# Performance work log

Measured on AMD Instinct MI355X. Metric: run time of the kernel, lower is better.

## Reference

```python
import jax, jax.numpy as jnp
import numpy as np
import itertools

NODE_DIM = 30
NUM_FEAT = 64
EDGE_DIM = NODE_DIM * NODE_DIM  # 900
D_IN, HID, LAT = 1024, 2048, 256
OUT_DIM = EDGE_DIM + NODE_DIM * NUM_FEAT  # 2820

_opt_nodes = [20, 21, 22, 23, 24, 25, 26, 27, 28, 29]
_opt_edges = [(i, j) for i, j in itertools.product(_opt_nodes, _opt_nodes) if i <= j]  # 55
_log_nodes = [20, 21, 22, 23, 24, 25, 26, 27, 28, 29, 14, 15]
_log_edges = [(i, j) for i, j in itertools.product(_log_nodes, _log_nodes) if i <= j]  # 78
N_OPT_NODES = len(_opt_nodes)          # 10
N_OPT_EDGES = len(_opt_edges)          # 55
N_LOG_NODES = len(_log_nodes)          # 12 (softmax width; only first 10 applied)
N_LOG_EDGES = len(_log_edges)          # 78 (softmax width; only first 55 applied)
OPT_NODES = jnp.array(_opt_nodes)
E0 = jnp.array([e[0] for e in _opt_edges])
E1 = jnp.array([e[1] for e in _opt_edges])


def _bn(x, g, b, m, v):
    # eval-mode BatchNorm1d, eps=1e-5
    return (x - m) * jax.lax.rsqrt(v + 1e-5) * g + b


def _attn_mlp(x, W1, b1, W2, b2):
    return jnp.tanh(x @ W1 + b1) @ W2 + b2


def _apply_attention(node_repr, edge_repr, node_w, edge_w):
    # softmax over full weight width, but indices always come from the optical lists
    nw = jax.nn.softmax(node_w, axis=1)[:, :N_OPT_NODES]   # [B,10]
    ew = jax.nn.softmax(edge_w, axis=1)[:, :N_OPT_EDGES]   # [B,55]
    node_repr = node_repr.at[:, OPT_NODES, :].set(node_repr[:, OPT_NODES, :] * nw[:, :, None])
    edge_repr = edge_repr.at[:, E0, E1].set(edge_repr[:, E0, E1] * ew)
    return node_repr, edge_repr


def setup_inputs() -> dict:
    key = jax.random.key(0)
    ks = iter(jax.random.split(key, 64))
    B = 8192
    s = 0.02
    def W(shape):
        return jax.random.normal(next(ks), shape, dtype=jnp.float32) * s
    inp = {
        "x": jax.random.normal(next(ks), (B, D_IN), dtype=jnp.float32),
        "optical": jax.random.normal(next(ks), (B, D_IN), dtype=jnp.float32),
        "log": jax.random.normal(next(ks), (B, D_IN), dtype=jnp.float32),
        "enc_W": W((D_IN, HID)), "enc_b": W((HID,)),
        "bn1_g": jnp.ones((HID,)), "bn1_b": jnp.zeros((HID,)),
        "bn1_m": W((HID,)), "bn1_v": jax.random.uniform(next(ks), (HID,)) + 0.5,
        "mu_W": W((HID, LAT)), "mu_b": W((LAT,)),
        "lv_W": W((HID, LAT)), "lv_b": W((LAT,)),
        "dec_W1": W((LAT, HID)), "dec_b1": W((HID,)),
        "bn2_g": jnp.ones((HID,)), "bn2_b": jnp.zeros((HID,)),
        "bn2_m": W((HID,)), "bn2_v": jax.random.uniform(next(ks), (HID,)) + 0.5,
        "dec_W2": W((HID, OUT_DIM)), "dec_b2": W((OUT_DIM,)),
        "on_W1": W((D_IN, D_IN // 2)), "on_b1": W((D_IN // 2,)),
        "on_W2": W((D_IN // 2, N_OPT_NODES)), "on_b2": W((N_OPT_NODES,)),
        "oe_W1": W((D_IN, D_IN // 2)), "oe_b1": W((D_IN // 2,)),
        "oe_W2": W((D_IN // 2, N_OPT_EDGES)), "oe_b2": W((N_OPT_EDGES,)),
        "ln_W1": W((D_IN, D_IN // 2)), "ln_b1": W((D_IN // 2,)),
        "ln_W2": W((D_IN // 2, N_LOG_NODES)), "ln_b2": W((N_LOG_NODES,)),
        "le_W1": W((D_IN, D_IN // 2)), "le_b1": W((D_IN // 2,)),
        "le_W2": W((D_IN // 2, N_LOG_EDGES)), "le_b2": W((N_LOG_EDGES,)),
    }
    return inp


def reference(x, optical, log, enc_W, enc_b, bn1_g, bn1_b, bn1_m, bn1_v,
              mu_W, mu_b, lv_W, lv_b, dec_W1, dec_b1, bn2_g, bn2_b, bn2_m, bn2_v,
              dec_W2, dec_b2, on_W1, on_b1, on_W2, on_b2, oe_W1, oe_b1, oe_W2, oe_b2,
              ln_W1, ln_b1, ln_W2, ln_b2, le_W1, le_b1, le_W2, le_b2):
    # encode (Linear -> ReLU -> BatchNorm(eval) -> Dropout(identity))
    h1 = _bn(jax.nn.relu(x @ enc_W + enc_b), bn1_g, bn1_b, bn1_m, bn1_v)
    mu = h1 @ mu_W + mu_b
    logvar = h1 @ lv_W + lv_b
    z = mu  # eval-mode reparameterize
    # decode
    h2 = _bn(jax.nn.relu(z @ dec_W1 + dec_b1), bn2_g, bn2_b, bn2_m, bn2_v)
    out = h2 @ dec_W2 + dec_b2
    edge_repr = out[:, :EDGE_DIM].reshape(-1, NODE_DIM, NODE_DIM)
    node_repr = out[:, EDGE_DIM:].reshape(-1, NODE_DIM, NUM_FEAT)
    # optical attention
    onw = _attn_mlp(optical, on_W1, on_b1, on_W2, on_b2)
    oew = _attn_mlp(optical, oe_W1, oe_b1, oe_W2, oe_b2)
    node_repr, edge_repr = _apply_attention(node_repr, edge_repr, onw, oew)
    # log attention (wider softmax, same indices — faithful to original code)
    lnw = _attn_mlp(log, ln_W1, ln_b1, ln_W2, ln_b2)
    lew = _attn_mlp(log, le_W1, le_b1, le_W2, le_b2)
    node_repr, edge_repr = _apply_attention(node_repr, edge_repr, lnw, lew)
    return edge_repr, node_repr, mu, logvar
```

## Files before the change

kernel.cpp:

```cpp
#include <hip/hip_runtime.h>

using u16 = unsigned short;
using u32 = unsigned int;

typedef __attribute__((ext_vector_type(8))) short bf16x8;
typedef __attribute__((ext_vector_type(4))) float f32x4;

#define MFMA16 __builtin_amdgcn_mfma_f32_16x16x32_bf16

__device__ __forceinline__ u16 f2bf(float f) {
  u32 u = __float_as_uint(f);
  u += 0x7fffu + ((u >> 16) & 1u);
  return (u16)(u >> 16);
}
__device__ __forceinline__ float bf2f(u16 h) { return __uint_as_float(((u32)h) << 16); }

__device__ __forceinline__ void gld16(const u16* g, u16* s) {
  __builtin_amdgcn_global_load_lds((const __attribute__((address_space(1))) u32*)g,
                                   (__attribute__((address_space(3))) u32*)s, 16, 0, 0);
}

struct EpParams {
  const float* bias;
  const float* bias2;
  const u16* b2;
  const float* bnsc;
  const float* bnsh;
  u16* dhi; u16* dlo; int dstride;
  float* f32a; float* f32b; int f32stride;
  const float* nscale; const float* escale;
};

template<int EP, int NM, bool SLO>
__global__ __launch_bounds__(256, (NM == 1) ? 3 : 2) void gemm_k(
    const u16* __restrict__ Ah, const u16* __restrict__ Al, int lda,
    const u16* __restrict__ Bh, const u16* __restrict__ Bl,
    int K, int N, EpParams p)
{
  __shared__ __align__(16) u16 sAh[4096], sBh[4096];
  __shared__ __align__(16) u16 sAl[(NM >= 2) ? 4096 : 16];
  __shared__ __align__(16) u16 sBl[(NM == 3) ? 4096 : 16];
  const int t = threadIdx.x;
  const int lane = t & 63, wid = t >> 6;
  const int tm = blockIdx.x, tn = blockIdx.y;

  const u16* BhS = Bh;
  const float* bias = p.bias;
  if constexpr (EP == 2 || EP == 5) {
    if (tm >= 64) { BhS = p.b2; bias = p.bias2; }
  }

  const int rp = t >> 2, sp = t & 3;
  const int rl = (rp & ~1) | ((rp & 1) ^ ((rp >> 2) & 1));
  const int sl = sp ^ (rl & 3);
  const u16* pAh = Ah + (size_t)(tm * 128 + rl) * (size_t)lda + sl * 8;
  const u16* pBh = BhS + (size_t)(tn * 128 + rl) * (size_t)K + sl * 8;
  const u16* pAl = (NM >= 2) ? Al + (size_t)(tm * 128 + rl) * (size_t)lda + sl * 8 : pAh;
  const u16* pBl = (NM == 3) ? Bl + (size_t)(tn * 128 + rl) * (size_t)K + sl * 8 : pBh;
  const size_t aStep = (size_t)64 * (size_t)lda;
  const size_t bStep = (size_t)64 * (size_t)K;

  f32x4 acc[4][4];
#pragma unroll
  for (int m = 0; m < 4; m++)
#pragma unroll
    for (int n = 0; n < 4; n++) acc[m][n] = f32x4{0.f, 0.f, 0.f, 0.f};

  const int fr = lane & 15, fg = lane >> 4;
  const int wm = wid >> 1, wn = wid & 1;

  for (int kk = 0; kk < K; kk += 32) {
    gld16(pAh + kk,          sAh + wid * 512);
    gld16(pAh + aStep + kk,  sAh + 2048 + wid * 512);
    gld16(pBh + kk,          sBh + wid * 512);
    gld16(pBh + bStep + kk,  sBh + 2048 + wid * 512);
    if constexpr (NM >= 2) {
      gld16(pAl + kk,         sAl + wid * 512);
      gld16(pAl + aStep + kk, sAl + 2048 + wid * 512);
    }
    if constexpr (NM == 3) {
      gld16(pBl + kk,         sBl + wid * 512);
      gld16(pBl + bStep + kk, sBl + 2048 + wid * 512);
    }
    __syncthreads();

    bf16x8 a_h[4], b_h[4], a_l[4], b_l[4];
#pragma unroll
    for (int f = 0; f < 4; f++) {
      const int ar = wm * 64 + f * 16 + fr;
      const int br = wn * 64 + f * 16 + fr;
      a_h[f] = *(const bf16x8*)&sAh[(ar * 32 + fg * 8) ^ ((ar & 7) << 3)];
      b_h[f] = *(const bf16x8*)&sBh[(br * 32 + fg * 8) ^ ((br & 7) << 3)];
      if constexpr (NM >= 2) a_l[f] = *(const bf16x8*)&sAl[(ar * 32 + fg * 8) ^ ((ar & 7) << 3)];
      if constexpr (NM == 3) b_l[f] = *(const bf16x8*)&sBl[(br * 32 + fg * 8) ^ ((br & 7) << 3)];
    }
#pragma unroll
    for (int m = 0; m < 4; m++)
#pragma unroll
      for (int n = 0; n < 4; n++) {
        if constexpr (NM == 3)
          acc[m][n] = MFMA16(a_h[m], b_l[n], acc[m][n], 0, 0, 0);
        if constexpr (NM >= 2)
          acc[m][n] = MFMA16(a_l[m], b_h[n], acc[m][n], 0, 0, 0);
        acc[m][n] = MFMA16(a_h[m], b_h[n], acc[m][n], 0, 0, 0);
      }
    __syncthreads();
  }

  const int rowb = tm * 128 + wm * 64;
  const int colb = tn * 128 + wn * 64;
#pragma unroll
  for (int n = 0; n < 4; n++) {
    const int col = colb + n * 16 + fr;
#pragma unroll
    for (int m = 0; m < 4; m++) {
#pragma unroll
      for (int r = 0; r < 4; r++) {
        const int row = rowb + m * 16 + fg * 4 + r;
        float val = acc[m][n][r];
        if constexpr (EP == 0) {
          val += bias[col];
          val = fmaxf(val, 0.f);
          val = val * p.bnsc[col] + p.bnsh[col];
          u16 h = f2bf(val);
          p.dhi[(size_t)row * p.dstride + col] = h;
          if constexpr (SLO)
            p.dlo[(size_t)row * p.dstride + col] = f2bf(val - bf2f(h));
        } else if constexpr (EP == 1) {
          val += bias[col];
          if (col < 256) {
            p.f32a[(size_t)row * 256 + col] = val;
            u16 h = f2bf(val);
            p.dhi[(size_t)row * 256 + col] = h;
            p.dlo[(size_t)row * 256 + col] = f2bf(val - bf2f(h));
          } else {
            p.f32b[(size_t)row * 256 + (col - 256)] = val;
          }
        } else if constexpr (EP == 2) {
          val = tanhf(val + bias[col]);
          p.dhi[(size_t)row * p.dstride + col] = f2bf(val);
        } else if constexpr (EP == 5) {
          if (tm < 64) {
            if (col < 65) p.f32a[(size_t)row * 65 + col] = val + bias[col];
          } else {
            if (col < 90) p.f32b[(size_t)(row - 8192) * 90 + col] = val + bias[col];
          }
        } else {
          if (col < N) {
            val += bias[col];
            if (col < 900) {
              int rr = col / 30, cc = col - rr * 30;
              float s = 1.f;
              if (rr >= 20 && cc >= 20 && rr <= cc) {
                int i0 = rr - 20, j0 = cc - 20;
                int k = i0 * 10 - ((i0 * (i0 - 1)) >> 1) + (j0 - i0);
                s = p.escale[(size_t)row * 55 + k];
              }
              p.f32a[(size_t)row * 900 + col] = val * s;
            } else {
              int tc = col - 900, rr = tc >> 6;
              float s = (rr >= 20) ? p.nscale[(size_t)row * 10 + (rr - 20)] : 1.f;
              p.f32b[(size_t)row * 1920 + tc] = val * s;
            }
          }
        }
      }
    }
  }
}

__global__ void conv3(const float* __restrict__ x, const float* __restrict__ opt,
                      const float* __restrict__ lg, u16* __restrict__ xh,
                      u16* __restrict__ xl, u16* __restrict__ oh, u16* __restrict__ lh) {
  const int SEG = 8192 * 1024 / 4;
  int i = blockIdx.x * blockDim.x + threadIdx.x;
  if (i < SEG) {
    float4 v = ((const float4*)x)[i];
    ushort4 hh, ll;
    hh.x = f2bf(v.x); ll.x = f2bf(v.x - bf2f(hh.x));
    hh.y = f2bf(v.y); ll.y = f2bf(v.y - bf2f(hh.y));
    hh.z = f2bf(v.z); ll.z = f2bf(v.z - bf2f(hh.z));
    hh.w = f2bf(v.w); ll.w = f2bf(v.w - bf2f(hh.w));
    ((ushort4*)xh)[i] = hh;
    ((ushort4*)xl)[i] = ll;
  } else if (i < 2 * SEG) {
    int j = i - SEG;
    float4 v = ((const float4*)opt)[j];
    ushort4 hh;
    hh.x = f2bf(v.x); hh.y = f2bf(v.y); hh.z = f2bf(v.z); hh.w = f2bf(v.w);
    ((ushort4*)oh)[j] = hh;
  } else if (i < 3 * SEG) {
    int j = i - 2 * SEG;
    float4 v = ((const float4*)lg)[j];
    ushort4 hh;
    hh.x = f2bf(v.x); hh.y = f2bf(v.y); hh.z = f2bf(v.z); hh.w = f2bf(v.w);
    ((ushort4*)lh)[j] = hh;
  }
}

struct WTJob { const float* src; u16* dh; int K, N, nbx, blk0; };
struct WTJobs { WTJob j[9]; };
__global__ void conv_wT_all(WTJobs J) {
  __shared__ float tile[32][33];
  const int b = blockIdx.x;
  int ji = 0;
#pragma unroll
  for (int q = 1; q < 9; q++) if (b >= J.j[q].blk0) ji = q;
  const WTJob jb = J.j[ji];
  const int bl = b - jb.blk0;
  const int kb = bl % jb.nbx, nb = bl / jb.nbx;
  const int k0 = kb * 32, n0 = nb * 32;
  const int tx = threadIdx.x, ty = threadIdx.y;
#pragma unroll
  for (int i = ty; i < 32; i += 8) {
    int n = n0 + tx;
    tile[i][tx] = (n < jb.N) ? jb.src[(size_t)(k0 + i) * jb.N + n] : 0.f;
  }
  __syncthreads();
#pragma unroll
  for (int i = ty; i < 32; i += 8) {
    int n = n0 + i, k = k0 + tx;
    jb.dh[(size_t)n * jb.K + k] = f2bf(tile[tx][i]);
  }
}

__global__ void conv_w2bd(const float* __restrict__ Wa, int Na,
                          const float* __restrict__ Wb, int Nb,
                          u16* __restrict__ Th) {
  int idx = blockIdx.x * blockDim.x + threadIdx.x;
  if (idx >= 128 * 1024) return;
  int n = idx >> 10, k = idx & 1023;
  float v = 0.f;
  if (n < Na) { if (k < 512) v = Wa[(size_t)k * Na + n]; }
  else if (n < Na + Nb) { if (k >= 512) v = Wb[(size_t)(k - 512) * Nb + (n - Na)]; }
  Th[idx] = f2bf(v);
}

struct PrepArgs {
  const float *bn1_g, *bn1_b, *bn1_m, *bn1_v, *bn2_g, *bn2_b, *bn2_m, *bn2_v;
  const float *mu_b, *lv_b, *on_b1, *oe_b1, *ln_b1, *le_b1, *on_b2, *oe_b2, *ln_b2, *le_b2;
  float *bn1sc, *bn1sh, *bn2sc, *bn2sh, *bias_mulv, *bias_o1, *bias_l1, *bias_o2, *bias_l2;
};
__global__ void prep_k(PrepArgs a) {
  int i = blockIdx.x * blockDim.x + threadIdx.x;
  if (i < 2048) {
    float s = a.bn1_g[i] * rsqrtf(a.bn1_v[i] + 1e-5f);
    a.bn1sc[i] = s; a.bn1sh[i] = a.bn1_b[i] - a.bn1_m[i] * s;
  } else if (i < 4096) {
    int j = i - 2048;
    float s = a.bn2_g[j] * rsqrtf(a.bn2_v[j] + 1e-5f);
    a.bn2sc[j] = s; a.bn2sh[j] = a.bn2_b[j] - a.bn2_m[j] * s;
  } else if (i < 4608) {
    int j = i - 4096; a.bias_mulv[j] = (j < 256) ? a.mu_b[j] : a.lv_b[j - 256];
  } else if (i < 5632) {
    int j = i - 4608; a.bias_o1[j] = (j < 512) ? a.on_b1[j] : a.oe_b1[j - 512];
  } else if (i < 6656) {
    int j = i - 5632; a.bias_l1[j] = (j < 512) ? a.ln_b1[j] : a.le_b1[j - 512];
  } else if (i < 6721) {
    int j = i - 6656; a.bias_o2[j] = (j < 10) ? a.on_b2[j] : a.oe_b2[j - 10];
  } else if (i < 6811) {
    int j = i - 6721; a.bias_l2[j] = (j < 12) ? a.ln_b2[j] : a.le_b2[j - 12];
  }
}

__global__ void softmax_combine(const float* __restrict__ lo, const float* __restrict__ ll,
                                float* __restrict__ nsc, float* __restrict__ esc) {
  int b = blockIdx.x * blockDim.x + threadIdx.x;
  if (b >= 8192) return;
  const float* po = lo + (size_t)b * 65;
  const float* pl = ll + (size_t)b * 90;
  float mo = po[0];
  for (int i = 1; i < 10; i++) mo = fmaxf(mo, po[i]);
  float so = 0.f;
  for (int i = 0; i < 10; i++) so += expf(po[i] - mo);
  float ml = pl[0];
  for (int i = 1; i < 12; i++) ml = fmaxf(ml, pl[i]);
  float sl = 0.f;
  for (int i = 0; i < 12; i++) sl += expf(pl[i] - ml);
  float invn = 1.f / (so * sl);
  for (int i = 0; i < 10; i++)
    nsc[(size_t)b * 10 + i] = expf(po[i] - mo) * expf(pl[i] - ml) * invn;
  const float* qo = po + 10;
  const float* ql = pl + 12;
  float meo = qo[0];
  for (int i = 1; i < 55; i++) meo = fmaxf(meo, qo[i]);
  float seo = 0.f;
  for (int i = 0; i < 55; i++) seo += expf(qo[i] - meo);
  float mel = ql[0];
  for (int i = 1; i < 78; i++) mel = fmaxf(mel, ql[i]);
  float sel = 0.f;
  for (int i = 0; i < 78; i++) sel += expf(ql[i] - mel);
  float inve = 1.f / (seo * sel);
  for (int k = 0; k < 55; k++)
    esc[(size_t)b * 55 + k] = expf(qo[k] - meo) * expf(ql[k] - mel) * inve;
}

extern "C" void kernel_launch(void* const* d_in, const int* in_sizes, int n_in,
                              void* d_out, int out_size, void* d_ws, size_t ws_size,
                              hipStream_t stream) {
  const float* x       = (const float*)d_in[0];
  const float* optical = (const float*)d_in[1];
  const float* logx    = (const float*)d_in[2];
  const float* enc_W   = (const float*)d_in[3];
  const float* enc_b   = (const float*)d_in[4];
  const float* bn1_g   = (const float*)d_in[5];
  const float* bn1_b   = (const float*)d_in[6];
  const float* bn1_m   = (const float*)d_in[7];
  const float* bn1_v   = (const float*)d_in[8];
  const float* mu_W    = (const float*)d_in[9];
  const float* mu_b    = (const float*)d_in[10];
  const float* lv_W    = (const float*)d_in[11];
  const float* lv_b    = (const float*)d_in[12];
  const float* dec_W1  = (const float*)d_in[13];
  const float* dec_b1  = (const float*)d_in[14];
  const float* bn2_g   = (const float*)d_in[15];
  const float* bn2_b   = (const float*)d_in[16];
  const float* bn2_m   = (const float*)d_in[17];
  const float* bn2_v   = (const float*)d_in[18];
  const float* dec_W2  = (const float*)d_in[19];
  const float* dec_b2  = (const float*)d_in[20];
  const float* on_W1   = (const float*)d_in[21];
  const float* on_b1   = (const float*)d_in[22];
  const float* on_W2   = (const float*)d_in[23];
  const float* on_b2   = (const float*)d_in[24];
  const float* oe_W1   = (const float*)d_in[25];
  const float* oe_b1   = (const float*)d_in[26];
  const float* oe_W2   = (const float*)d_in[27];
  const float* oe_b2   = (const float*)d_in[28];
  const float* ln_W1   = (const float*)d_in[29];
  const float* ln_b1   = (const float*)d_in[30];
  const float* ln_W2   = (const float*)d_in[31];
  const float* ln_b2   = (const float*)d_in[32];
  const float* le_W1   = (const float*)d_in[33];
  const float* le_b1   = (const float*)d_in[34];
  const float* le_W2   = (const float*)d_in[35];
  const float* le_b2   = (const float*)d_in[36];

  const int B = 8192;
  float* out_edge = (float*)d_out;
  float* out_node = out_edge + (size_t)B * 900;
  float* out_mu   = out_node + (size_t)B * 1920;
  float* out_lv   = out_mu + (size_t)B * 256;

  char* base = (char*)d_ws;
  size_t off = 0;
  auto takeB = [&](size_t elems) -> u16* {
    u16* p = (u16*)(base + off);
    off = (off + elems * 2 + 255) & ~(size_t)255;
    return p;
  };
  auto takeF = [&](size_t elems) -> float* {
    float* p = (float*)(base + off);
    off = (off + elems * 4 + 255) & ~(size_t)255;
    return p;
  };
  u16* wEncH  = takeB(2048 * 1024);
  u16* wMulvH = takeB(512 * 2048);
  u16* wDec1H = takeB(2048 * 256);
  u16* wDec2H = takeB(2944 * 2048);
  u16* wO1H   = takeB(1024 * 1024);
  u16* wL1H   = takeB(1024 * 1024);
  u16* wO2H   = takeB(128 * 1024);
  u16* wL2H   = takeB(128 * 1024);
  u16* aXh = takeB((size_t)B * 1024); u16* aXl = takeB((size_t)B * 1024);
  u16* aOLh = takeB((size_t)2 * B * 1024);
  u16* aOh = aOLh;
  u16* aLh = aOLh + (size_t)B * 1024;
  u16* aHh = takeB((size_t)B * 2048); u16* aHl = takeB((size_t)B * 2048);
  u16* aZh = takeB((size_t)B * 256);  u16* aZl = takeB((size_t)B * 256);
  u16* aTh = takeB((size_t)2 * B * 1024);
  float* logitsO = takeF((size_t)B * 65);
  float* logitsL = takeF((size_t)B * 90);
  float* nsc = takeF((size_t)B * 10);
  float* esc = takeF((size_t)B * 55);
  float* bn1sc = takeF(2048); float* bn1sh = takeF(2048);
  float* bn2sc = takeF(2048); float* bn2sh = takeF(2048);
  float* bias_mulv = takeF(512);
  float* bias_o1 = takeF(1024);
  float* bias_l1 = takeF(1024);
  float* bias_o2 = takeF(65);
  float* bias_l2 = takeF(90);

  PrepArgs pa;
  pa.bn1_g = bn1_g; pa.bn1_b = bn1_b; pa.bn1_m = bn1_m; pa.bn1_v = bn1_v;
  pa.bn2_g = bn2_g; pa.bn2_b = bn2_b; pa.bn2_m = bn2_m; pa.bn2_v = bn2_v;
  pa.mu_b = mu_b; pa.lv_b = lv_b;
  pa.on_b1 = on_b1; pa.oe_b1 = oe_b1; pa.ln_b1 = ln_b1; pa.le_b1 = le_b1;
  pa.on_b2 = on_b2; pa.oe_b2 = oe_b2; pa.ln_b2 = ln_b2; pa.le_b2 = le_b2;
  pa.bn1sc = bn1sc; pa.bn1sh = bn1sh; pa.bn2sc = bn2sc; pa.bn2sh = bn2sh;
  pa.bias_mulv = bias_mulv; pa.bias_o1 = bias_o1; pa.bias_l1 = bias_l1;
  pa.bias_o2 = bias_o2; pa.bias_l2 = bias_l2;
  prep_k<<<27, 256, 0, stream>>>(pa);

  conv3<<<24576, 256, 0, stream>>>(x, optical, logx, aXh, aXl, aOh, aLh);

  WTJobs wj;
  int blk = 0;
  auto addjob = [&](int idx, const float* src, u16* dh, int K, int N, int Npad) {
    wj.j[idx] = WTJob{src, dh, K, N, K / 32, blk};
    blk += (K / 32) * (Npad / 32);
  };
  addjob(0, enc_W,  wEncH,  1024, 2048, 2048);
  addjob(1, mu_W,   wMulvH, 2048, 256, 256);
  addjob(2, lv_W,   wMulvH + (size_t)256 * 2048, 2048, 256, 256);
  addjob(3, dec_W1, wDec1H, 256, 2048, 2048);
  addjob(4, dec_W2, wDec2H, 2048, 2820, 2944);
  addjob(5, on_W1,  wO1H,                        1024, 512, 512);
  addjob(6, oe_W1,  wO1H + (size_t)512 * 1024,   1024, 512, 512);
  addjob(7, ln_W1,  wL1H,                        1024, 512, 512);
  addjob(8, le_W1,  wL1H + (size_t)512 * 1024,   1024, 512, 512);
  conv_wT_all<<<blk, dim3(32, 8), 0, stream>>>(wj);
  conv_w2bd<<<512, 256, 0, stream>>>(on_W2, 10, oe_W2, 55, wO2H);
  conv_w2bd<<<512, 256, 0, stream>>>(ln_W2, 12, le_W2, 78, wL2H);

  EpParams p;

  p = EpParams{};
  p.bias = enc_b; p.bnsc = bn1sc; p.bnsh = bn1sh;
  p.dhi = aHh; p.dlo = aHl; p.dstride = 2048;
  gemm_k<0, 2, true><<<dim3(64, 16), 256, 0, stream>>>(
      aXh, aXl, 1024, wEncH, nullptr, 1024, 2048, p);

  p = EpParams{};
  p.bias = bias_mulv; p.f32a = out_mu; p.f32b = out_lv;
  p.dhi = aZh; p.dlo = aZl; p.dstride = 256;
  gemm_k<1, 2, false><<<dim3(64, 4), 256, 0, stream>>>(
      aHh, aHl, 2048, wMulvH, nullptr, 2048, 512, p);

  p = EpParams{};
  p.bias = dec_b1; p.bnsc = bn2sc; p.bnsh = bn2sh;
  p.dhi = aHh; p.dlo = nullptr; p.dstride = 2048;
  gemm_k<0, 2, false><<<dim3(64, 16), 256, 0, stream>>>(
      aZh, aZl, 256, wDec1H, nullptr, 256, 2048, p);

  p = EpParams{};
  p.bias = bias_o1; p.bias2 = bias_l1; p.b2 = wL1H;
  p.dhi = aTh; p.dstride = 1024;
  gemm_k<2, 1, false><<<dim3(128, 8), 256, 0, stream>>>(
      aOLh, nullptr, 1024, wO1H, nullptr, 1024, 1024, p);

  p = EpParams{};
  p.bias = bias_o2; p.bias2 = bias_l2; p.b2 = wL2H;
  p.f32a = logitsO; p.f32b = logitsL;
  gemm_k<5, 1, false><<<dim3(128, 1), 256, 0, stream>>>(
      aTh, nullptr, 1024, wO2H, nullptr, 1024, 128, p);

  softmax_combine<<<32, 256, 0, stream>>>(logitsO, logitsL, nsc, esc);

  p = EpParams{};
  p.bias = dec_b2; p.nscale = nsc; p.escale = esc;
  p.f32a = out_edge; p.f32b = out_node;
  gemm_k<4, 1, false><<<dim3(64, 23), 256, 0, stream>>>(
      aHh, nullptr, 2048, wDec2H, nullptr, 2048, 2820, p);
}
```

Before: 786.0 us.

## Merge prep kernels and co-schedule independent GEMMs in combined launches

Folds the input conversion, weight transposes, block-diagonal weight packing and bias/BN prep into a single launch. It also runs independent GEMMs inside one grid: the encoder with the first attention MLP layer, mu/logvar with the second attention layer, and decoder layer 1 with the softmax. The goal is to cut launch overhead and fill the GPU with work from independent stages at the same time. The cost is that the combined kernels always allocate three LDS buffers and use a shared launch-bounds setting, which may reduce occupancy for the single-matrix GEMM paths.

```diff
diff --git a/kernel.cpp b/kernel.cpp
--- a/kernel.cpp
+++ b/kernel.cpp
@@ -31,32 +31,34 @@
   const float* nscale; const float* escale;
 };
 
+struct GemmJob {
+  const u16* Ah; const u16* Al; int lda;
+  const u16* Bh;
+  int K, N, ntm;
+  EpParams p;
+};
+
 template<int EP, int NM, bool SLO>
-__global__ __launch_bounds__(256, (NM == 1) ? 3 : 2) void gemm_k(
-    const u16* __restrict__ Ah, const u16* __restrict__ Al, int lda,
-    const u16* __restrict__ Bh, const u16* __restrict__ Bl,
-    int K, int N, EpParams p)
-{
-  __shared__ __align__(16) u16 sAh[4096], sBh[4096];
-  __shared__ __align__(16) u16 sAl[(NM >= 2) ? 4096 : 16];
-  __shared__ __align__(16) u16 sBl[(NM == 3) ? 4096 : 16];
+__device__ __forceinline__ void gemm_body(const GemmJob& J, int lbid,
+                                          u16* sAh, u16* sBh, u16* sAl) {
+  const EpParams& p = J.p;
   const int t = threadIdx.x;
   const int lane = t & 63, wid = t >> 6;
-  const int tm = blockIdx.x, tn = blockIdx.y;
-
-  const u16* BhS = Bh;
+  const int tm = lbid % J.ntm, tn = lbid / J.ntm;
+  const int K = J.K, lda = J.lda;
+
+  const u16* BhS = J.Bh;
   const float* bias = p.bias;
   if constexpr (EP == 2 || EP == 5) {
-    if (tm >= 64) { BhS = p.b2; bias = p.bias2; }
+    if (tm >= (J.ntm >> 1)) { BhS = p.b2; bias = p.bias2; }
   }
 
   const int rp = t >> 2, sp = t & 3;
   const int rl = (rp & ~1) | ((rp & 1) ^ ((rp >> 2) & 1));
   const int sl = sp ^ (rl & 3);
-  const u16* pAh = Ah + (size_t)(tm * 128 + rl) * (size_t)lda + sl * 8;
+  const u16* pAh = J.Ah + (size_t)(tm * 128 + rl) * (size_t)lda + sl * 8;
   const u16* pBh = BhS + (size_t)(tn * 128 + rl) * (size_t)K + sl * 8;
-  const u16* pAl = (NM >= 2) ? Al + (size_t)(tm * 128 + rl) * (size_t)lda + sl * 8 : pAh;
-  const u16* pBl = (NM == 3) ? Bl + (size_t)(tn * 128 + rl) * (size_t)K + sl * 8 : pBh;
+  const u16* pAl = (NM >= 2) ? J.Al + (size_t)(tm * 128 + rl) * (size_t)lda + sl * 8 : pAh;
   const size_t aStep = (size_t)64 * (size_t)lda;
   const size_t bStep = (size_t)64 * (size_t)K;
 
@@ -78,13 +80,9 @@
       gld16(pAl + kk,         sAl + wid * 512);
       gld16(pAl + aStep + kk, sAl + 2048 + wid * 512);
     }
-    if constexpr (NM == 3) {
-      gld16(pBl + kk,         sBl + wid * 512);
-      gld16(pBl + bStep + kk, sBl + 2048 + wid * 512);
-    }
     __syncthreads();
 
-    bf16x8 a_h[4], b_h[4], a_l[4], b_l[4];
+    bf16x8 a_h[4], b_h[4], a_l[4];
 #pragma unroll
     for (int f = 0; f < 4; f++) {
       const int ar = wm * 64 + f * 16 + fr;
@@ -92,14 +90,11 @@
       a_h[f] = *(const bf16x8*)&sAh[(ar * 32 + fg * 8) ^ ((ar & 7) << 3)];
       b_h[f] = *(const bf16x8*)&sBh[(br * 32 + fg * 8) ^ ((br & 7) << 3)];
       if constexpr (NM >= 2) a_l[f] = *(const bf16x8*)&sAl[(ar * 32 + fg * 8) ^ ((ar & 7) << 3)];
-      if constexpr (NM == 3) b_l[f] = *(const bf16x8*)&sBl[(br * 32 + fg * 8) ^ ((br & 7) << 3)];
     }
 #pragma unroll
     for (int m = 0; m < 4; m++)
 #pragma unroll
       for (int n = 0; n < 4; n++) {
-        if constexpr (NM == 3)
-          acc[m][n] = MFMA16(a_h[m], b_l[n], acc[m][n], 0, 0, 0);
         if constexpr (NM >= 2)
           acc[m][n] = MFMA16(a_l[m], b_h[n], acc[m][n], 0, 0, 0);
         acc[m][n] = MFMA16(a_h[m], b_h[n], acc[m][n], 0, 0, 0);
@@ -146,7 +141,7 @@
             if (col < 90) p.f32b[(size_t)(row - 8192) * 90 + col] = val + bias[col];
           }
         } else {
-          if (col < N) {
+          if (col < J.N) {
             val += bias[col];
             if (col < 900) {
               int rr = col / 30, cc = col - rr * 30;
@@ -169,106 +164,18 @@
   }
 }
 
-__global__ void conv3(const float* __restrict__ x, const float* __restrict__ opt,
-                      const float* __restrict__ lg, u16* __restrict__ xh,
-                      u16* __restrict__ xl, u16* __restrict__ oh, u16* __restrict__ lh) {
-  const int SEG = 8192 * 1024 / 4;
-  int i = blockIdx.x * blockDim.x + threadIdx.x;
-  if (i < SEG) {
-    float4 v = ((const float4*)x)[i];
-    ushort4 hh, ll;
-    hh.x = f2bf(v.x); ll.x = f2bf(v.x - bf2f(hh.x));
-    hh.y = f2bf(v.y); ll.y = f2bf(v.y - bf2f(hh.y));
-    hh.z = f2bf(v.z); ll.z = f2bf(v.z - bf2f(hh.z));
-    hh.w = f2bf(v.w); ll.w = f2bf(v.w - bf2f(hh.w));
-    ((ushort4*)xh)[i] = hh;
-    ((ushort4*)xl)[i] = ll;
-  } else if (i < 2 * SEG) {
-    int j = i - SEG;
-    float4 v = ((const float4*)opt)[j];
-    ushort4 hh;
-    hh.x = f2bf(v.x); hh.y = f2bf(v.y); hh.z = f2bf(v.z); hh.w = f2bf(v.w);
-    ((ushort4*)oh)[j] = hh;
-  } else if (i < 3 * SEG) {
-    int j = i - 2 * SEG;
-    float4 v = ((const float4*)lg)[j];
-    ushort4 hh;
-    hh.x = f2bf(v.x); hh.y = f2bf(v.y); hh.z = f2bf(v.z); hh.w = f2bf(v.w);
-    ((ushort4*)lh)[j] = hh;
-  }
-}
-
-struct WTJob { const float* src; u16* dh; int K, N, nbx, blk0; };
-struct WTJobs { WTJob j[9]; };
-__global__ void conv_wT_all(WTJobs J) {
-  __shared__ float tile[32][33];
-  const int b = blockIdx.x;
-  int ji = 0;
-#pragma unroll
-  for (int q = 1; q < 9; q++) if (b >= J.j[q].blk0) ji = q;
-  const WTJob jb = J.j[ji];
-  const int bl = b - jb.blk0;
-  const int kb = bl % jb.nbx, nb = bl / jb.nbx;
-  const int k0 = kb * 32, n0 = nb * 32;
-  const int tx = threadIdx.x, ty = threadIdx.y;
-#pragma unroll
-  for (int i = ty; i < 32; i += 8) {
-    int n = n0 + tx;
-    tile[i][tx] = (n < jb.N) ? jb.src[(size_t)(k0 + i) * jb.N + n] : 0.f;
-  }
-  __syncthreads();
-#pragma unroll
-  for (int i = ty; i < 32; i += 8) {
-    int n = n0 + i, k = k0 + tx;
-    jb.dh[(size_t)n * jb.K + k] = f2bf(tile[tx][i]);
-  }
-}
-
-__global__ void conv_w2bd(const float* __restrict__ Wa, int Na,
-                          const float* __restrict__ Wb, int Nb,
-                          u16* __restrict__ Th) {
-  int idx = blockIdx.x * blockDim.x + threadIdx.x;
-  if (idx >= 128 * 1024) return;
-  int n = idx >> 10, k = idx & 1023;
-  float v = 0.f;
-  if (n < Na) { if (k < 512) v = Wa[(size_t)k * Na + n]; }
-  else if (n < Na + Nb) { if (k >= 512) v = Wb[(size_t)(k - 512) * Nb + (n - Na)]; }
-  Th[idx] = f2bf(v);
-}
-
-struct PrepArgs {
-  const float *bn1_g, *bn1_b, *bn1_m, *bn1_v, *bn2_g, *bn2_b, *bn2_m, *bn2_v;
-  const float *mu_b, *lv_b, *on_b1, *oe_b1, *ln_b1, *le_b1, *on_b2, *oe_b2, *ln_b2, *le_b2;
-  float *bn1sc, *bn1sh, *bn2sc, *bn2sh, *bias_mulv, *bias_o1, *bias_l1, *bias_o2, *bias_l2;
-};
-__global__ void prep_k(PrepArgs a) {
-  int i = blockIdx.x * blockDim.x + threadIdx.x;
-  if (i < 2048) {
-    float s = a.bn1_g[i] * rsqrtf(a.bn1_v[i] + 1e-5f);
-    a.bn1sc[i] = s; a.bn1sh[i] = a.bn1_b[i] - a.bn1_m[i] * s;
-  } else if (i < 4096) {
-    int j = i - 2048;
-    float s = a.bn2_g[j] * rsqrtf(a.bn2_v[j] + 1e-5f);
-    a.bn2sc[j] = s; a.bn2sh[j] = a.bn2_b[j] - a.bn2_m[j] * s;
-  } else if (i < 4608) {
-    int j = i - 4096; a.bias_mulv[j] = (j < 256) ? a.mu_b[j] : a.lv_b[j - 256];
-  } else if (i < 5632) {
-    int j = i - 4608; a.bias_o1[j] = (j < 512) ? a.on_b1[j] : a.oe_b1[j - 512];
-  } else if (i < 6656) {
-    int j = i - 5632; a.bias_l1[j] = (j < 512) ? a.ln_b1[j] : a.le_b1[j - 512];
-  } else if (i < 6721) {
-    int j = i - 6656; a.bias_o2[j] = (j < 10) ? a.on_b2[j] : a.oe_b2[j - 10];
-  } else if (i < 6811) {
-    int j = i - 6721; a.bias_l2[j] = (j < 12) ? a.ln_b2[j] : a.le_b2[j - 12];
-  }
-}
-
-__global__ void softmax_combine(const float* __restrict__ lo, const float* __restrict__ ll,
-                                float* __restrict__ nsc, float* __restrict__ esc) {
-  int b = blockIdx.x * blockDim.x + threadIdx.x;
+template<int EP, int NM, bool SLO>
+__global__ __launch_bounds__(256, (NM == 1) ? 3 : 2) void gemm_k(GemmJob J) {
+  __shared__ __align__(16) u16 sAh[4096], sBh[4096];
+  gemm_body<EP, NM, SLO>(J, blockIdx.x, sAh, sBh, sAh );
+}
+
+struct SmaxArgs { const float* lo; const float* ll; float* nsc; float* esc; };
+
+__device__ __forceinline__ void softmax_body(const SmaxArgs& a, int b) {
   if (b >= 8192) return;
-  const float* po = lo + (size_t)b * 65;
-  const float* pl = ll + (size_t)b * 90;
+  const float* po = a.lo + (size_t)b * 65;
+  const float* pl = a.ll + (size_t)b * 90;
   float mo = po[0];
   for (int i = 1; i < 10; i++) mo = fmaxf(mo, po[i]);
   float so = 0.f;
@@ -279,7 +186,7 @@
   for (int i = 0; i < 12; i++) sl += expf(pl[i] - ml);
   float invn = 1.f / (so * sl);
   for (int i = 0; i < 10; i++)
-    nsc[(size_t)b * 10 + i] = expf(po[i] - mo) * expf(pl[i] - ml) * invn;
+    a.nsc[(size_t)b * 10 + i] = expf(po[i] - mo) * expf(pl[i] - ml) * invn;
   const float* qo = po + 10;
   const float* ql = pl + 12;
   float meo = qo[0];
@@ -292,7 +199,121 @@
   for (int i = 0; i < 78; i++) sel += expf(ql[i] - mel);
   float inve = 1.f / (seo * sel);
   for (int k = 0; k < 55; k++)
-    esc[(size_t)b * 55 + k] = expf(qo[k] - meo) * expf(ql[k] - mel) * inve;
+    a.esc[(size_t)b * 55 + k] = expf(qo[k] - meo) * expf(ql[k] - mel) * inve;
+}
+
+template<int EPA, int NMA, bool SLOA, int EPB, int NMB, bool SLOB, bool SMAX>
+__global__ __launch_bounds__(256, 2) void super_k(
+    int splitA, int splitB, GemmJob ja, GemmJob jb, SmaxArgs sm) {
+  __shared__ __align__(16) u16 sAh[4096], sBh[4096], sAl[4096];
+  const int bid = blockIdx.x;
+  if (bid < splitA) {
+    gemm_body<EPA, NMA, SLOA>(ja, bid, sAh, sBh, sAl);
+  } else if (bid < splitB) {
+    gemm_body<EPB, NMB, SLOB>(jb, bid - splitA, sAh, sBh, sAl);
+  } else if constexpr (SMAX) {
+    softmax_body(sm, (bid - splitB) * 256 + threadIdx.x);
+  }
+}
+
+struct WTJob { const float* src; u16* dh; int K, N, nbx, blk0; };
+struct PrepArgs {
+  const float *bn1_g, *bn1_b, *bn1_m, *bn1_v, *bn2_g, *bn2_b, *bn2_m, *bn2_v;
+  const float *mu_b, *lv_b, *on_b1, *oe_b1, *ln_b1, *le_b1, *on_b2, *oe_b2, *ln_b2, *le_b2;
+  float *bn1sc, *bn1sh, *bn2sc, *bn2sh, *bias_mulv, *bias_o1, *bias_l1, *bias_o2, *bias_l2;
+};
+struct MegaArgs {
+  const float *x, *opt, *lg; u16 *xh, *xl, *oh, *lh;
+  WTJob wt[9];
+  int wt_base, bd_base, prep_base;
+  const float *onW2, *oeW2, *lnW2, *leW2; u16 *o2T, *l2T;
+  PrepArgs pr;
+};
+
+__global__ void mega_prep(MegaArgs A) {
+  const int bid = blockIdx.x;
+  const int t = threadIdx.x;
+  if (bid < A.wt_base) {
+    const int SEG = 8192 * 1024 / 4;
+    int i = bid * 256 + t;
+    if (i < SEG) {
+      float4 v = ((const float4*)A.x)[i];
+      ushort4 hh, ll;
+      hh.x = f2bf(v.x); ll.x = f2bf(v.x - bf2f(hh.x));
+      hh.y = f2bf(v.y); ll.y = f2bf(v.y - bf2f(hh.y));
+      hh.z = f2bf(v.z); ll.z = f2bf(v.z - bf2f(hh.z));
+      hh.w = f2bf(v.w); ll.w = f2bf(v.w - bf2f(hh.w));
+      ((ushort4*)A.xh)[i] = hh;
+      ((ushort4*)A.xl)[i] = ll;
+    } else if (i < 2 * SEG) {
+      int j = i - SEG;
+      float4 v = ((const float4*)A.opt)[j];
+      ushort4 hh;
+      hh.x = f2bf(v.x); hh.y = f2bf(v.y); hh.z = f2bf(v.z); hh.w = f2bf(v.w);
+      ((ushort4*)A.oh)[j] = hh;
+    } else {
+      int j = i - 2 * SEG;
+      float4 v = ((const float4*)A.lg)[j];
+      ushort4 hh;
+      hh.x = f2bf(v.x); hh.y = f2bf(v.y); hh.z = f2bf(v.z); hh.w = f2bf(v.w);
+      ((ushort4*)A.lh)[j] = hh;
+    }
+  } else if (bid < A.bd_base) {
+    __shared__ float tile[32][33];
+    const int b = bid - A.wt_base;
+    int ji = 0;
+#pragma unroll
+    for (int q = 1; q < 9; q++) if (b >= A.wt[q].blk0) ji = q;
+    const WTJob jb = A.wt[ji];
+    const int bl = b - jb.blk0;
+    const int k0 = (bl % jb.nbx) * 32, n0 = (bl / jb.nbx) * 32;
+    const int tx = t & 31, ty = t >> 5;
+#pragma unroll
+    for (int i = ty; i < 32; i += 8) {
+      int n = n0 + tx;
+      tile[i][tx] = (n < jb.N) ? jb.src[(size_t)(k0 + i) * jb.N + n] : 0.f;
+    }
+    __syncthreads();
+#pragma unroll
+    for (int i = ty; i < 32; i += 8) {
+      int n = n0 + i, k = k0 + tx;
+      jb.dh[(size_t)n * jb.K + k] = f2bf(tile[tx][i]);
+    }
+  } else if (bid < A.prep_base) {
+    const int lb = bid - A.bd_base;
+    const bool second = lb >= 512;
+    const int idx = (second ? lb - 512 : lb) * 256 + t;
+    const float* Wa = second ? A.lnW2 : A.onW2;
+    const float* Wb = second ? A.leW2 : A.oeW2;
+    u16* Th = second ? A.l2T : A.o2T;
+    const int Na = second ? 12 : 10, Nb = second ? 78 : 55;
+    int n = idx >> 10, k = idx & 1023;
+    float v = 0.f;
+    if (n < Na) { if (k < 512) v = Wa[(size_t)k * Na + n]; }
+    else if (n < Na + Nb) { if (k >= 512) v = Wb[(size_t)(k - 512) * Nb + (n - Na)]; }
+    Th[idx] = f2bf(v);
+  } else {
+    const PrepArgs& a = A.pr;
+    int i = (bid - A.prep_base) * 256 + t;
+    if (i < 2048) {
+      float s = a.bn1_g[i] * rsqrtf(a.bn1_v[i] + 1e-5f);
+      a.bn1sc[i] = s; a.bn1sh[i] = a.bn1_b[i] - a.bn1_m[i] * s;
+    } else if (i < 4096) {
+      int j = i - 2048;
+      float s = a.bn2_g[j] * rsqrtf(a.bn2_v[j] + 1e-5f);
+      a.bn2sc[j] = s; a.bn2sh[j] = a.bn2_b[j] - a.bn2_m[j] * s;
+    } else if (i < 4608) {
+      int j = i - 4096; a.bias_mulv[j] = (j < 256) ? a.mu_b[j] : a.lv_b[j - 256];
+    } else if (i < 5632) {
+      int j = i - 4608; a.bias_o1[j] = (j < 512) ? a.on_b1[j] : a.oe_b1[j - 512];
+    } else if (i < 6656) {
+      int j = i - 5632; a.bias_l1[j] = (j < 512) ? a.ln_b1[j] : a.le_b1[j - 512];
+    } else if (i < 6721) {
+      int j = i - 6656; a.bias_o2[j] = (j < 10) ? a.on_b2[j] : a.oe_b2[j - 10];
+    } else if (i < 6811) {
+      int j = i - 6721; a.bias_l2[j] = (j < 12) ? a.ln_b2[j] : a.le_b2[j - 12];
+    }
+  }
 }
 
 extern "C" void kernel_launch(void* const* d_in, const int* in_sizes, int n_in,
@@ -381,23 +402,12 @@
   float* bias_o2 = takeF(65);
   float* bias_l2 = takeF(90);
 
-  PrepArgs pa;
-  pa.bn1_g = bn1_g; pa.bn1_b = bn1_b; pa.bn1_m = bn1_m; pa.bn1_v = bn1_v;
-  pa.bn2_g = bn2_g; pa.bn2_b = bn2_b; pa.bn2_m = bn2_m; pa.bn2_v = bn2_v;
-  pa.mu_b = mu_b; pa.lv_b = lv_b;
-  pa.on_b1 = on_b1; pa.oe_b1 = oe_b1; pa.ln_b1 = ln_b1; pa.le_b1 = le_b1;
-  pa.on_b2 = on_b2; pa.oe_b2 = oe_b2; pa.ln_b2 = ln_b2; pa.le_b2 = le_b2;
-  pa.bn1sc = bn1sc; pa.bn1sh = bn1sh; pa.bn2sc = bn2sc; pa.bn2sh = bn2sh;
-  pa.bias_mulv = bias_mulv; pa.bias_o1 = bias_o1; pa.bias_l1 = bias_l1;
-  pa.bias_o2 = bias_o2; pa.bias_l2 = bias_l2;
-  prep_k<<<27, 256, 0, stream>>>(pa);
-
-  conv3<<<24576, 256, 0, stream>>>(x, optical, logx, aXh, aXl, aOh, aLh);
-
-  WTJobs wj;
+  MegaArgs ma;
+  ma.x = x; ma.opt = optical; ma.lg = logx;
+  ma.xh = aXh; ma.xl = aXl; ma.oh = aOh; ma.lh = aLh;
   int blk = 0;
   auto addjob = [&](int idx, const float* src, u16* dh, int K, int N, int Npad) {
-    wj.j[idx] = WTJob{src, dh, K, N, K / 32, blk};
+    ma.wt[idx] = WTJob{src, dh, K, N, K / 32, blk};
     blk += (K / 32) * (Npad / 32);
   };
   addjob(0, enc_W,  wEncH,  1024, 2048, 2048);
@@ -409,47 +419,71 @@
   addjob(6, oe_W1,  wO1H + (size_t)512 * 1024,   1024, 512, 512);
   addjob(7, ln_W1,  wL1H,                        1024, 512, 512);
   addjob(8, le_W1,  wL1H + (size_t)512 * 1024,   1024, 512, 512);
-  conv_wT_all<<<blk, dim3(32, 8), 0, stream>>>(wj);
-  conv_w2bd<<<512, 256, 0, stream>>>(on_W2, 10, oe_W2, 55, wO2H);
-  conv_w2bd<<<512, 256, 0, stream>>>(ln_W2, 12, le_W2, 78, wL2H);
-
-  EpParams p;
-
-  p = EpParams{};
-  p.bias = enc_b; p.bnsc = bn1sc; p.bnsh = bn1sh;
-  p.dhi = aHh; p.dlo = aHl; p.dstride = 2048;
-  gemm_k<0, 2, true><<<dim3(64, 16), 256, 0, stream>>>(
-      aXh, aXl, 1024, wEncH, nullptr, 1024, 2048, p);
-
-  p = EpParams{};
-  p.bias = bias_mulv; p.f32a = out_mu; p.f32b = out_lv;
-  p.dhi = aZh; p.dlo = aZl; p.dstride = 256;
-  gemm_k<1, 2, false><<<dim3(64, 4), 256, 0, stream>>>(
-      aHh, aHl, 2048, wMulvH, nullptr, 2048, 512, p);
-
-  p = EpParams{};
-  p.bias = dec_b1; p.bnsc = bn2sc; p.bnsh = bn2sh;
-  p.dhi = aHh; p.dlo = nullptr; p.dstride = 2048;
-  gemm_k<0, 2, false><<<dim3(64, 16), 256, 0, stream>>>(
-      aZh, aZl, 256, wDec1H, nullptr, 256, 2048, p);
-
-  p = EpParams{};
-  p.bias = bias_o1; p.bias2 = bias_l1; p.b2 = wL1H;
-  p.dhi = aTh; p.dstride = 1024;
-  gemm_k<2, 1, false><<<dim3(128, 8), 256, 0, stream>>>(
-      aOLh, nullptr, 1024, wO1H, nullptr, 1024, 1024, p);
-
-  p = EpParams{};
-  p.bias = bias_o2; p.bias2 = bias_l2; p.b2 = wL2H;
-  p.f32a = logitsO; p.f32b = logitsL;
-  gemm_k<5, 1, false><<<dim3(128, 1), 256, 0, stream>>>(
-      aTh, nullptr, 1024, wO2H, nullptr, 1024, 128, p);
-
-  softmax_combine<<<32, 256, 0, stream>>>(logitsO, logitsL, nsc, esc);
-
-  p = EpParams{};
-  p.bias = dec_b2; p.nscale = nsc; p.escale = esc;
-  p.f32a = out_edge; p.f32b = out_node;
-  gemm_k<4, 1, false><<<dim3(64, 23), 256, 0, stream>>>(
-      aHh, nullptr, 2048, wDec2H, nullptr, 2048, 2820, p);
-}
+  const int CONV3_BLOCKS = 24576;
+  ma.wt_base = CONV3_BLOCKS;
+  ma.bd_base = CONV3_BLOCKS + blk;
+  ma.prep_base = ma.bd_base + 1024;
+  ma.onW2 = on_W2; ma.oeW2 = oe_W2; ma.lnW2 = ln_W2; ma.leW2 = le_W2;
+  ma.o2T = wO2H; ma.l2T = wL2H;
+  PrepArgs& pa = ma.pr;
+  pa.bn1_g = bn1_g; pa.bn1_b = bn1_b; pa.bn1_m = bn1_m; pa.bn1_v = bn1_v;
+  pa.bn2_g = bn2_g; pa.bn2_b = bn2_b; pa.bn2_m = bn2_m; pa.bn2_v = bn2_v;
+  pa.mu_b = mu_b; pa.lv_b = lv_b;
+  pa.on_b1 = on_b1; pa.oe_b1 = oe_b1; pa.ln_b1 = ln_b1; pa.le_b1 = le_b1;
+  pa.on_b2 = on_b2; pa.oe_b2 = oe_b2; pa.ln_b2 = ln_b2; pa.le_b2 = le_b2;
+  pa.bn1sc = bn1sc; pa.bn1sh = bn1sh; pa.bn2sc = bn2sc; pa.bn2sh = bn2sh;
+  pa.bias_mulv = bias_mulv; pa.bias_o1 = bias_o1; pa.bias_l1 = bias_l1;
+  pa.bias_o2 = bias_o2; pa.bias_l2 = bias_l2;
+  mega_prep<<<ma.prep_base + 27, 256, 0, stream>>>(ma);
+
+  SmaxArgs smnull{nullptr, nullptr, nullptr, nullptr};
+  GemmJob jnull{};
+
+  GemmJob jEnc;
+  jEnc.Ah = aXh; jEnc.Al = aXl; jEnc.lda = 1024; jEnc.Bh = wEncH;
+  jEnc.K = 1024; jEnc.N = 2048; jEnc.ntm = 64;
+  jEnc.p = EpParams{};
+  jEnc.p.bias = enc_b; jEnc.p.bnsc = bn1sc; jEnc.p.bnsh = bn1sh;
+  jEnc.p.dhi = aHh; jEnc.p.dlo = aHl; jEnc.p.dstride = 2048;
+  GemmJob jA1;
+  jA1.Ah = aOLh; jA1.Al = nullptr; jA1.lda = 1024; jA1.Bh = wO1H;
+  jA1.K = 1024; jA1.N = 1024; jA1.ntm = 128;
+  jA1.p = EpParams{};
+  jA1.p.bias = bias_o1; jA1.p.bias2 = bias_l1; jA1.p.b2 = wL1H;
+  jA1.p.dhi = aTh; jA1.p.dstride = 1024;
+  super_k<0, 2, true, 2, 1, false, false><<<1024 + 1024, 256, 0, stream>>>(
+      1024, 2048, jEnc, jA1, smnull);
+
+  GemmJob jMulv;
+  jMulv.Ah = aHh; jMulv.Al = aHl; jMulv.lda = 2048; jMulv.Bh = wMulvH;
+  jMulv.K = 2048; jMulv.N = 512; jMulv.ntm = 64;
+  jMulv.p = EpParams{};
+  jMulv.p.bias = bias_mulv; jMulv.p.f32a = out_mu; jMulv.p.f32b = out_lv;
+  jMulv.p.dhi = aZh; jMulv.p.dlo = aZl; jMulv.p.dstride = 256;
+  GemmJob jA2;
+  jA2.Ah = aTh; jA2.Al = nullptr; jA2.lda = 1024; jA2.Bh = wO2H;
+  jA2.K = 1024; jA2.N = 128; jA2.ntm = 128;
+  jA2.p = EpParams{};
+  jA2.p.bias = bias_o2; jA2.p.bias2 = bias_l2; jA2.p.b2 = wL2H;
+  jA2.p.f32a = logitsO; jA2.p.f32b = logitsL;
+  super_k<1, 2, false, 5, 1, false, false><<<256 + 128, 256, 0, stream>>>(
+      256, 384, jMulv, jA2, smnull);
+
+  GemmJob jD1;
+  jD1.Ah = aZh; jD1.Al = aZl; jD1.lda = 256; jD1.Bh = wDec1H;
+  jD1.K = 256; jD1.N = 2048; jD1.ntm = 64;
+  jD1.p = EpParams{};
+  jD1.p.bias = dec_b1; jD1.p.bnsc = bn2sc; jD1.p.bnsh = bn2sh;
+  jD1.p.dhi = aHh; jD1.p.dlo = nullptr; jD1.p.dstride = 2048;
+  SmaxArgs sm{logitsO, logitsL, nsc, esc};
+  super_k<0, 2, false, 0, 1, false, true><<<1024 + 32, 256, 0, stream>>>(
+      1024, 1024, jD1, jnull, sm);
+
+  GemmJob jD2;
+  jD2.Ah = aHh; jD2.Al = nullptr; jD2.lda = 2048; jD2.Bh = wDec2H;
+  jD2.K = 2048; jD2.N = 2820; jD2.ntm = 64;
+  jD2.p = EpParams{};
+  jD2.p.bias = dec_b2; jD2.p.nscale = nsc; jD2.p.escale = esc;
+  jD2.p.f32a = out_edge; jD2.p.f32b = out_node;
+  gemm_k<4, 1, false><<<64 * 23, 256, 0, stream>>>(jD2);
+}
```

Measured after the change: 773.1 us. Within noise of the previous version (-1.6%).
